# Optimization experiments

Hardware: AMD Instinct MI355X
Metric: run time of the kernel (lower is better)

The kernel has to match this reference:

```python
import jax, jax.numpy as jnp
import numpy as np

N_HEAD = 16

def _ln(x, g, b):
    m = jnp.mean(x, axis=-1, keepdims=True)
    v = jnp.var(x, axis=-1, keepdims=True)
    return (x - m) / jnp.sqrt(v + 1e-5) * g + b

def setup_inputs() -> dict:
    key = jax.random.key(0)
    B, T, D, L, V = 2, 1024, 1024, 4, 32000
    ks = jax.random.split(key, 8)
    s = 0.02
    return {
        'input_ids': jax.random.randint(ks[0], (B, T), 0, V),
        'wte': jax.random.normal(ks[1], (V, D), jnp.float32) * s,
        'wpe': jax.random.normal(ks[2], (T, D), jnp.float32) * s,
        'ln1_g': jnp.ones((L, D), jnp.float32), 'ln1_b': jnp.zeros((L, D), jnp.float32),
        'w_qkv': jax.random.normal(ks[3], (L, D, 3 * D), jnp.float32) * s,
        'b_qkv': jnp.zeros((L, 3 * D), jnp.float32),
        'w_proj': jax.random.normal(ks[4], (L, D, D), jnp.float32) * s,
        'b_proj': jnp.zeros((L, D), jnp.float32),
        'ln2_g': jnp.ones((L, D), jnp.float32), 'ln2_b': jnp.zeros((L, D), jnp.float32),
        'w_fc1': jax.random.normal(ks[5], (L, D, 4 * D), jnp.float32) * s,
        'b_fc1': jnp.zeros((L, 4 * D), jnp.float32),
        'w_fc2': jax.random.normal(ks[6], (L, 4 * D, D), jnp.float32) * s,
        'b_fc2': jnp.zeros((L, D), jnp.float32),
        'lnf_g': jnp.ones((D,), jnp.float32), 'lnf_b': jnp.zeros((D,), jnp.float32),
        'w_lm': jax.random.normal(ks[7], (D, V), jnp.float32) * s,
    }

def reference(input_ids, wte, wpe, ln1_g, ln1_b, w_qkv, b_qkv, w_proj, b_proj,
              ln2_g, ln2_b, w_fc1, b_fc1, w_fc2, b_fc2, lnf_g, lnf_b, w_lm):
    B, T = input_ids.shape
    D = wte.shape[1]
    H = N_HEAD
    hd = D // H
    mask = jnp.tril(jnp.ones((T, T), dtype=bool))  # causal
    x = wte[input_ids] + wpe[:T][None, :, :]  # token + position embeddings

    def layer(h, p):
        g1, bb1, Wq, bq, Wp, bp, g2, bb2, W1, b1, W2, b2 = p
        a = _ln(h, g1, bb1)
        qkv = a @ Wq + bq
        q, k, v = jnp.split(qkv, 3, axis=-1)
        q = q.reshape(B, T, H, hd)
        k = k.reshape(B, T, H, hd)
        v = v.reshape(B, T, H, hd)
        att = jnp.einsum('bqhd,bkhd->bhqk', q, k) / jnp.sqrt(jnp.float32(hd))
        att = jnp.where(mask[None, None], att, -jnp.inf)
        att = jax.nn.softmax(att, axis=-1)
        y = jnp.einsum('bhqk,bkhd->bqhd', att, v).reshape(B, T, D)
        h = h + y @ Wp + bp
        m = _ln(h, g2, bb2)
        # torch nn.GELU default is exact erf variant
        m = jax.nn.gelu(m @ W1 + b1, approximate=False) @ W2 + b2
        h = h + m
        return h, None

    params = (ln1_g, ln1_b, w_qkv, b_qkv, w_proj, b_proj,
              ln2_g, ln2_b, w_fc1, b_fc1, w_fc2, b_fc2)
    h, _ = jax.lax.scan(layer, x, params)
    h = _ln(h, lnf_g, lnf_b)
    logits = h @ w_lm  # [B, T, vocab]
    return logits
```

## Files before the change

### kernel.cpp

```cpp
#include <hip/hip_runtime.h>
#include <hip/hip_bf16.h>
#include <math.h>

typedef __attribute__((ext_vector_type(4))) float f32x4;
typedef __attribute__((ext_vector_type(8))) short short8;
typedef __attribute__((ext_vector_type(4))) unsigned short ushort4v;

__device__ __forceinline__ unsigned short f2bf(float f) {
    return __builtin_bit_cast(unsigned short, __float2bfloat16(f));
}

__device__ __forceinline__ void gload16(const void* g, void* l) {
    __builtin_amdgcn_global_load_lds(
        (const __attribute__((address_space(1))) unsigned int*)g,
        (__attribute__((address_space(3))) unsigned int*)l, 16, 0, 0);
}

__global__ __launch_bounds__(256)
void tc_kernel(const float* __restrict__ in, __hip_bfloat16* __restrict__ out,
               int N, int K)
{
    __shared__ float tile[64][65];
    const size_t loff = (size_t)blockIdx.z * K * N;
    const int k0 = blockIdx.x * 64, n0 = blockIdx.y * 64;
    const int t = threadIdx.x;
    {
        int kk = t >> 2, nb = (t & 3) * 16;
        const float* src = in + loff + (size_t)(k0 + kk) * N + n0 + nb;
        #pragma unroll
        for (int j = 0; j < 4; ++j) {
            float4 v = *(const float4*)(src + j * 4);
            tile[kk][nb + j*4 + 0] = v.x; tile[kk][nb + j*4 + 1] = v.y;
            tile[kk][nb + j*4 + 2] = v.z; tile[kk][nb + j*4 + 3] = v.w;
        }
    }
    __syncthreads();
    {
        int nn = t >> 2, kb = (t & 3) * 16;
        __hip_bfloat16* dst = out + loff + (size_t)(n0 + nn) * K + k0 + kb;
        short8 w0, w1;
        #pragma unroll
        for (int j = 0; j < 8; ++j) w0[j] = (short)f2bf(tile[kb + j][nn]);
        #pragma unroll
        for (int j = 0; j < 8; ++j) w1[j] = (short)f2bf(tile[kb + 8 + j][nn]);
        *(short8*)dst = w0;
        *(short8*)(dst + 8) = w1;
    }
}

__global__ __launch_bounds__(256)
void embed_kernel(const int* __restrict__ ids, const float* __restrict__ wte,
                  const float* __restrict__ wpe, float* __restrict__ h)
{
    int row  = blockIdx.x;
    int tpos = row & 1023;
    int id   = ids[row];
    float4 a = ((const float4*)(wte + (size_t)id * 1024))[threadIdx.x];
    float4 p = ((const float4*)(wpe + (size_t)tpos * 1024))[threadIdx.x];
    float4 o; o.x = a.x + p.x; o.y = a.y + p.y; o.z = a.z + p.z; o.w = a.w + p.w;
    ((float4*)(h + (size_t)row * 1024))[threadIdx.x] = o;
}

__global__ __launch_bounds__(256)
void ln_kernel(const float* __restrict__ x, const float* __restrict__ g,
               const float* __restrict__ b, __hip_bfloat16* __restrict__ out)
{
    size_t row = blockIdx.x;
    float4 v = ((const float4*)(x + row * 1024))[threadIdx.x];
    float s  = v.x + v.y + v.z + v.w;
    float s2 = v.x*v.x + v.y*v.y + v.z*v.z + v.w*v.w;
    #pragma unroll
    for (int off = 32; off; off >>= 1) {
        s  += __shfl_xor(s, off);
        s2 += __shfl_xor(s2, off);
    }
    __shared__ float rs[4], rs2[4];
    int wave = threadIdx.x >> 6;
    if ((threadIdx.x & 63) == 0) { rs[wave] = s; rs2[wave] = s2; }
    __syncthreads();
    s  = rs[0] + rs[1] + rs[2] + rs[3];
    s2 = rs2[0] + rs2[1] + rs2[2] + rs2[3];
    float mean = s * (1.f / 1024.f);
    float var  = s2 * (1.f / 1024.f) - mean * mean;
    float rstd = rsqrtf(var + 1e-5f);
    float4 gg = ((const float4*)g)[threadIdx.x];
    float4 bb = ((const float4*)b)[threadIdx.x];
    ushort4v ov;
    ov[0] = f2bf((v.x - mean) * rstd * gg.x + bb.x);
    ov[1] = f2bf((v.y - mean) * rstd * gg.y + bb.y);
    ov[2] = f2bf((v.z - mean) * rstd * gg.z + bb.z);
    ov[3] = f2bf((v.w - mean) * rstd * gg.w + bb.w);
    ((ushort4v*)(out + row * 1024))[threadIdx.x] = ov;
}

template<bool OUT_BF16, bool GELU_ACT, bool NT, int BN>
__global__ __launch_bounds__(256)
void gemm_bf16(const __hip_bfloat16* __restrict__ A,
               const __hip_bfloat16* __restrict__ Bt,
               const float* __restrict__ bias, const float* __restrict__ resid,
               void* __restrict__ Cout, int M, int N, int K, int GN)
{
    __shared__ unsigned char smem[32768 + 2 * BN * 128];
    int mblk, pnl;
    {
        int bid = blockIdx.x;
        int x = bid & 7, j = bid >> 3;
        int pw = GN >> 3;
        int whole = pw * 128;
        if (bid < whole) { pnl = x + 8 * (j >> 4); mblk = j & 15; }
        else { int r = bid - whole; pnl = (pw << 3) + (r >> 4); mblk = r & 15; }
    }
    const int m0 = mblk * 128;
    const int n0 = pnl * BN;
    const int t    = threadIdx.x;
    const int lane = t & 63;
    const int wave = t >> 6;
    constexpr int NF = (BN == 128) ? 4 : 2;
    const int wm = (BN == 128) ? (wave >> 1) * 64 : (wave & 1) * 64;
    const int wn = (BN == 128) ? (wave & 1) * 64 : (wave >> 1) * 32;

    f32x4 acc[4][NF];
    #pragma unroll
    for (int i = 0; i < 4; ++i)
        #pragma unroll
        for (int j = 0; j < NF; ++j) {
            acc[i][j][0] = 0.f; acc[i][j][1] = 0.f; acc[i][j][2] = 0.f; acc[i][j][3] = 0.f;
        }

    const int l8 = lane >> 3;
    const int lc = (lane & 7) ^ l8;
    constexpr int NB = NF;
    const __hip_bfloat16* agp[4];
    const __hip_bfloat16* bgp[NB];
    int aoff[4];
    int boff[NB];
    #pragma unroll
    for (int i = 0; i < 4; ++i) {
        int row = wave * 32 + i * 8 + l8;
        agp[i]  = A + (size_t)(m0 + row) * K + lc * 8;
        aoff[i] = (wave * 32 + i * 8) * 128;
    }
    #pragma unroll
    for (int i = 0; i < NB; ++i) {
        int row = wave * (BN / 4) + i * 8 + l8;
        bgp[i]  = Bt + (size_t)(n0 + row) * K + lc * 8;
        boff[i] = (wave * (BN / 4) + i * 8) * 128;
    }
    const int aBufOff[2] = { 0, 16384 };
    const int bBufOff[2] = { 32768, 32768 + BN * 128 };

    #pragma unroll
    for (int i = 0; i < 4; ++i)  gload16(agp[i], smem + aBufOff[0] + aoff[i]);
    #pragma unroll
    for (int i = 0; i < NB; ++i) gload16(bgp[i], smem + bBufOff[0] + boff[i]);
    __syncthreads();

    int cur = 0;
    for (int k0 = 0; k0 < K; k0 += 64) {
        if (k0 + 64 < K) {
            #pragma unroll
            for (int i = 0; i < 4; ++i)
                gload16(agp[i] + k0 + 64, smem + aBufOff[cur ^ 1] + aoff[i]);
            #pragma unroll
            for (int i = 0; i < NB; ++i)
                gload16(bgp[i] + k0 + 64, smem + bBufOff[cur ^ 1] + boff[i]);
        }
        const unsigned char* abuf = smem + aBufOff[cur];
        const unsigned char* bbuf = smem + bBufOff[cur];
        const int lr = lane & 15;
        const int lk = lane >> 4;
        #pragma unroll
        for (int ks = 0; ks < 2; ++ks) {
            int chunk = ks * 4 + lk;
            short8 af[4], bfr[NF];
            #pragma unroll
            for (int m = 0; m < 4; ++m) {
                int row = wm + m * 16 + lr;
                af[m] = *(const short8*)(abuf + row * 128 + ((chunk * 16) ^ ((row & 7) << 4)));
            }
            #pragma unroll
            for (int n = 0; n < NF; ++n) {
                int nn = wn + n * 16 + lr;
                bfr[n] = *(const short8*)(bbuf + nn * 128 + ((chunk * 16) ^ ((nn & 7) << 4)));
            }
            #pragma unroll
            for (int m = 0; m < 4; ++m)
                #pragma unroll
                for (int n = 0; n < NF; ++n)
                    acc[m][n] = __builtin_amdgcn_mfma_f32_16x16x32_bf16(af[m], bfr[n], acc[m][n], 0, 0, 0);
        }
        __syncthreads();
        cur ^= 1;
    }

    const int lr = lane & 15;
    const int lq = lane >> 4;
    float bv[NF];
    #pragma unroll
    for (int n = 0; n < NF; ++n)
        bv[n] = bias ? bias[n0 + wn + n * 16 + lr] : 0.f;
    #pragma unroll
    for (int m = 0; m < 4; ++m) {
        int rbase = m0 + wm + m * 16 + lq * 4;
        #pragma unroll
        for (int j = 0; j < 4; ++j) {
            int row = rbase + j;
            #pragma unroll
            for (int n = 0; n < NF; ++n) {
                int col = n0 + wn + n * 16 + lr;
                float v = acc[m][n][j] + bv[n];
                if (resid) v += resid[(size_t)row * N + col];
                if (GELU_ACT) v = 0.5f * v * (1.f + erff(v * 0.70710678118654752f));
                if (OUT_BF16) {
                    ((__hip_bfloat16*)Cout)[(size_t)row * N + col] = __float2bfloat16(v);
                } else if (NT) {
                    __builtin_nontemporal_store(v, (float*)Cout + (size_t)row * N + col);
                } else {
                    ((float*)Cout)[(size_t)row * N + col] = v;
                }
            }
        }
    }
}

__global__ __launch_bounds__(256)
void attn_mfma(const __hip_bfloat16* __restrict__ qkv,
               __hip_bfloat16* __restrict__ y)
{
    __shared__ short Qs[64][72];
    __shared__ short Ps[64][72];
    __shared__ unsigned char Kl[8192];
    __shared__ short Vt[64][72];

    const int bid = blockIdx.x;
    const int p   = bid >> 5;
    const int qt  = (p < 8) ? (15 - 2 * p) : (2 * (p - 8));
    const int bh  = bid & 31;
    const int b = bh >> 4, h = bh & 15;
    const int t = threadIdx.x, lane = t & 63, w = t >> 6;
    const int lr = lane & 15, lg = lane >> 4;
    const size_t base = (size_t)b * 1024 * 3072;
    const int qbase = qt * 64;

    {
        int row = t >> 2, c = t & 3;
        const short8* qsrc = (const short8*)(qkv + base + (size_t)(qbase + row) * 3072 + h * 64);
        *(short8*)&Qs[row][c * 8]      = qsrc[c];
        *(short8*)&Qs[row][c * 8 + 32] = qsrc[c + 4];
    }
    __syncthreads();

    short8 aq0 = *(const short8*)&Qs[w * 16 + lr][0 * 32 + lg * 8];
    short8 aq1 = *(const short8*)&Qs[w * 16 + lr][1 * 32 + lg * 8];

    f32x4 oacc[4];
    #pragma unroll
    for (int dt = 0; dt < 4; ++dt) { oacc[dt][0]=0.f; oacc[dt][1]=0.f; oacc[dt][2]=0.f; oacc[dt][3]=0.f; }
    float lsum[4] = {0.f, 0.f, 0.f, 0.f};

    const int ntiles = qt + 1;
    const int kkey = t >> 2, kc = t & 3;
    const int vkey = t & 63, vc = t >> 6;

    short8 rk0, rk1, rv0, rv1;
    {
        const short8* ksrc = (const short8*)(qkv + base + (size_t)kkey * 3072 + 1024 + h * 64);
        rk0 = ksrc[kc]; rk1 = ksrc[kc + 4];
        const short8* vsrc = (const short8*)(qkv + base + (size_t)vkey * 3072 + 2048 + h * 64);
        rv0 = vsrc[vc]; rv1 = vsrc[vc + 4];
    }
    {
        int rb = kkey * 128, sw = (kkey & 7) << 4;
        *(short8*)(Kl + rb + ((kc * 16) ^ sw)) = rk0;
        *(short8*)(Kl + rb + (((kc + 4) * 16) ^ sw)) = rk1;
        #pragma unroll
        for (int j = 0; j < 8; ++j) Vt[vc * 8 + j][vkey] = rv0[j];
        #pragma unroll
        for (int j = 0; j < 8; ++j) Vt[(vc + 4) * 8 + j][vkey] = rv1[j];
    }
    __syncthreads();

    for (int tile = 0; tile < ntiles; ++tile) {
        if (tile + 1 < ntiles) {
            const int kb2 = (tile + 1) * 64;
            const short8* ksrc = (const short8*)(qkv + base + (size_t)(kb2 + kkey) * 3072 + 1024 + h * 64);
            rk0 = ksrc[kc]; rk1 = ksrc[kc + 4];
            const short8* vsrc = (const short8*)(qkv + base + (size_t)(kb2 + vkey) * 3072 + 2048 + h * 64);
            rv0 = vsrc[vc]; rv1 = vsrc[vc + 4];
        }

        const int kb = tile * 64;
        f32x4 sacc[4];
        #pragma unroll
        for (int kt = 0; kt < 4; ++kt) { sacc[kt][0]=0.f; sacc[kt][1]=0.f; sacc[kt][2]=0.f; sacc[kt][3]=0.f; }
        #pragma unroll
        for (int ks = 0; ks < 2; ++ks) {
            short8 aq = ks ? aq1 : aq0;
            #pragma unroll
            for (int kt = 0; kt < 4; ++kt) {
                int krow = kt * 16 + lr;
                short8 bk = *(const short8*)(Kl + krow * 128 + (((ks * 4 + lg) * 16) ^ ((krow & 7) << 4)));
                sacc[kt] = __builtin_amdgcn_mfma_f32_16x16x32_bf16(aq, bk, sacc[kt], 0, 0, 0);
            }
        }

        #pragma unroll
        for (int kt = 0; kt < 4; ++kt) {
            int key = kb + kt * 16 + lr;
            #pragma unroll
            for (int j = 0; j < 4; ++j) {
                int q = qbase + w * 16 + lg * 4 + j;
                float pv = (key <= q) ? __expf(sacc[kt][j] * 0.125f) : 0.f;
                lsum[j] += pv;
                Ps[w * 16 + lg * 4 + j][kt * 16 + lr] = (short)f2bf(pv);
            }
        }

        #pragma unroll
        for (int ks = 0; ks < 2; ++ks) {
            short8 ap = *(const short8*)&Ps[w * 16 + lr][ks * 32 + lg * 8];
            #pragma unroll
            for (int dt = 0; dt < 4; ++dt) {
                short8 bv = *(const short8*)&Vt[dt * 16 + lr][ks * 32 + lg * 8];
                oacc[dt] = __builtin_amdgcn_mfma_f32_16x16x32_bf16(ap, bv, oacc[dt], 0, 0, 0);
            }
        }

        if (tile + 1 < ntiles) {
            __syncthreads();
            int rb = kkey * 128, sw = (kkey & 7) << 4;
            *(short8*)(Kl + rb + ((kc * 16) ^ sw)) = rk0;
            *(short8*)(Kl + rb + (((kc + 4) * 16) ^ sw)) = rk1;
            #pragma unroll
            for (int j = 0; j < 8; ++j) Vt[vc * 8 + j][vkey] = rv0[j];
            #pragma unroll
            for (int j = 0; j < 8; ++j) Vt[(vc + 4) * 8 + j][vkey] = rv1[j];
            __syncthreads();
        }
    }

    #pragma unroll
    for (int j = 0; j < 4; ++j) {
        float l = lsum[j];
        l += __shfl_xor(l, 1); l += __shfl_xor(l, 2);
        l += __shfl_xor(l, 4); l += __shfl_xor(l, 8);
        float inv = 1.f / l;
        int qrow = qbase + w * 16 + lg * 4 + j;
        __hip_bfloat16* dst = y + (size_t)(b * 1024 + qrow) * 1024 + h * 64;
        #pragma unroll
        for (int dt = 0; dt < 4; ++dt)
            dst[dt * 16 + lr] = __float2bfloat16(oacc[dt][j] * inv);
    }
}

extern "C" void kernel_launch(void* const* d_in, const int* in_sizes, int n_in,
                              void* d_out, int out_size, void* d_ws, size_t ws_size,
                              hipStream_t stream)
{
    (void)in_sizes; (void)n_in; (void)out_size; (void)ws_size;

    const int*   ids    = (const int*)d_in[0];
    const float* wte    = (const float*)d_in[1];
    const float* wpe    = (const float*)d_in[2];
    const float* ln1_g  = (const float*)d_in[3];
    const float* ln1_b  = (const float*)d_in[4];
    const float* w_qkv  = (const float*)d_in[5];
    const float* b_qkv  = (const float*)d_in[6];
    const float* w_proj = (const float*)d_in[7];
    const float* b_proj = (const float*)d_in[8];
    const float* ln2_g  = (const float*)d_in[9];
    const float* ln2_b  = (const float*)d_in[10];
    const float* w_fc1  = (const float*)d_in[11];
    const float* b_fc1  = (const float*)d_in[12];
    const float* w_fc2  = (const float*)d_in[13];
    const float* b_fc2  = (const float*)d_in[14];
    const float* lnf_g  = (const float*)d_in[15];
    const float* lnf_b  = (const float*)d_in[16];
    const float* w_lm   = (const float*)d_in[17];

    char* ws = (char*)d_ws;
    __hip_bfloat16* abuf_bf = (__hip_bfloat16*)ws;
    float*          hbuf    = (float*)(ws + (4u<<20));
    __hip_bfloat16* qkvb_bf = (__hip_bfloat16*)(ws + (12u<<20));
    __hip_bfloat16* ybuf_bf = (__hip_bfloat16*)(ws + (24u<<20));
    __hip_bfloat16* mbuf_bf = (__hip_bfloat16*)(ws + (28u<<20));
    __hip_bfloat16* wlm_bf  = (__hip_bfloat16*)(ws + (4u<<20));

    __hip_bfloat16* wq_bf = (__hip_bfloat16*)d_out;
    __hip_bfloat16* wp_bf = wq_bf + (size_t)4*1024*3072;
    __hip_bfloat16* w1_bf = wp_bf + (size_t)4*1024*1024;
    __hip_bfloat16* w2_bf = w1_bf + (size_t)4*1024*4096;

    float* out = (float*)d_out;

    tc_kernel<<<dim3(16, 48, 4), 256, 0, stream>>>(w_qkv,  wq_bf, 3072, 1024);
    tc_kernel<<<dim3(16, 16, 4), 256, 0, stream>>>(w_proj, wp_bf, 1024, 1024);
    tc_kernel<<<dim3(16, 64, 4), 256, 0, stream>>>(w_fc1,  w1_bf, 4096, 1024);
    tc_kernel<<<dim3(64, 16, 4), 256, 0, stream>>>(w_fc2,  w2_bf, 1024, 4096);

    embed_kernel<<<2048, 256, 0, stream>>>(ids, wte, wpe, hbuf);

    for (int l = 0; l < 4; ++l) {
        ln_kernel<<<2048, 256, 0, stream>>>(hbuf, ln1_g + l*1024, ln1_b + l*1024, abuf_bf);
        gemm_bf16<true,false,false,128><<<16*24, 256, 0, stream>>>(
            abuf_bf, wq_bf + (size_t)l*1024*3072, b_qkv + l*3072, nullptr, qkvb_bf, 2048, 3072, 1024, 24);
        attn_mfma<<<512, 256, 0, stream>>>(qkvb_bf, ybuf_bf);
        gemm_bf16<false,false,false,64><<<16*16, 256, 0, stream>>>(
            ybuf_bf, wp_bf + (size_t)l*1024*1024, b_proj + l*1024, hbuf, hbuf, 2048, 1024, 1024, 16);
        ln_kernel<<<2048, 256, 0, stream>>>(hbuf, ln2_g + l*1024, ln2_b + l*1024, abuf_bf);
        gemm_bf16<true,true,false,128><<<16*32, 256, 0, stream>>>(
            abuf_bf, w1_bf + (size_t)l*1024*4096, b_fc1 + l*4096, nullptr, mbuf_bf, 2048, 4096, 1024, 32);
        gemm_bf16<false,false,false,64><<<16*16, 256, 0, stream>>>(
            mbuf_bf, w2_bf + (size_t)l*4096*1024, b_fc2 + l*1024, hbuf, hbuf, 2048, 1024, 4096, 16);
    }

    ln_kernel<<<2048, 256, 0, stream>>>(hbuf, lnf_g, lnf_b, abuf_bf);
    tc_kernel<<<dim3(16, 500, 1), 256, 0, stream>>>(w_lm, wlm_bf, 32000, 1024);
    gemm_bf16<false,false,true,128><<<16*250, 256, 0, stream>>>(
        abuf_bf, wlm_bf, nullptr, nullptr, out, 2048, 32000, 1024, 250);
}
```

Measured before the change: 893.8 us.

## Triple-buffer GEMM LDS pipeline and use 128x64 tiles for all GEMMs

Switches the bf16 GEMM from double-buffered to triple-buffered LDS staging with two tiles in flight. Each iteration waits on vmcnt and issues one barrier instead of a full __syncthreads after compute. It also drops the BN=128 variant, so the QKV, FC1 and LM-head GEMMs now use 128x64 tiles with twice as many blocks. This should hide global-load latency better and raise block count, but LDS use grows to 72KB per block, which may lower occupancy. The narrower tiles also give less reuse of A per block.

```diff
diff --git a/kernel.cpp b/kernel.cpp
--- a/kernel.cpp
+++ b/kernel.cpp
@@ -15,6 +15,9 @@
         (const __attribute__((address_space(1))) unsigned int*)g,
         (__attribute__((address_space(3))) unsigned int*)l, 16, 0, 0);
 }
+
+#define WAITV6() asm volatile("s_waitcnt vmcnt(6)" ::: "memory")
+#define WAITV0() asm volatile("s_waitcnt vmcnt(0)" ::: "memory")
 
 __global__ __launch_bounds__(256)
 void tc_kernel(const float* __restrict__ in, __hip_bfloat16* __restrict__ out,
@@ -93,14 +96,14 @@
     ((ushort4v*)(out + row * 1024))[threadIdx.x] = ov;
 }
 
-template<bool OUT_BF16, bool GELU_ACT, bool NT, int BN>
+template<bool OUT_BF16, bool GELU_ACT, bool NT>
 __global__ __launch_bounds__(256)
 void gemm_bf16(const __hip_bfloat16* __restrict__ A,
                const __hip_bfloat16* __restrict__ Bt,
                const float* __restrict__ bias, const float* __restrict__ resid,
                void* __restrict__ Cout, int M, int N, int K, int GN)
 {
-    __shared__ unsigned char smem[32768 + 2 * BN * 128];
+    __shared__ unsigned char smem[73728];
     int mblk, pnl;
     {
         int bid = blockIdx.x;
@@ -111,29 +114,27 @@
         else { int r = bid - whole; pnl = (pw << 3) + (r >> 4); mblk = r & 15; }
     }
     const int m0 = mblk * 128;
-    const int n0 = pnl * BN;
+    const int n0 = pnl * 64;
     const int t    = threadIdx.x;
     const int lane = t & 63;
     const int wave = t >> 6;
-    constexpr int NF = (BN == 128) ? 4 : 2;
-    const int wm = (BN == 128) ? (wave >> 1) * 64 : (wave & 1) * 64;
-    const int wn = (BN == 128) ? (wave & 1) * 64 : (wave >> 1) * 32;
-
-    f32x4 acc[4][NF];
+    const int wm = (wave & 1) * 64;
+    const int wn = (wave >> 1) * 32;
+
+    f32x4 acc[4][2];
     #pragma unroll
     for (int i = 0; i < 4; ++i)
         #pragma unroll
-        for (int j = 0; j < NF; ++j) {
+        for (int j = 0; j < 2; ++j) {
             acc[i][j][0] = 0.f; acc[i][j][1] = 0.f; acc[i][j][2] = 0.f; acc[i][j][3] = 0.f;
         }
 
     const int l8 = lane >> 3;
     const int lc = (lane & 7) ^ l8;
-    constexpr int NB = NF;
     const __hip_bfloat16* agp[4];
-    const __hip_bfloat16* bgp[NB];
+    const __hip_bfloat16* bgp[2];
     int aoff[4];
-    int boff[NB];
+    int boff[2];
     #pragma unroll
     for (int i = 0; i < 4; ++i) {
         int row = wave * 32 + i * 8 + l8;
@@ -141,63 +142,68 @@
         aoff[i] = (wave * 32 + i * 8) * 128;
     }
     #pragma unroll
-    for (int i = 0; i < NB; ++i) {
-        int row = wave * (BN / 4) + i * 8 + l8;
+    for (int i = 0; i < 2; ++i) {
+        int row = wave * 16 + i * 8 + l8;
         bgp[i]  = Bt + (size_t)(n0 + row) * K + lc * 8;
-        boff[i] = (wave * (BN / 4) + i * 8) * 128;
-    }
-    const int aBufOff[2] = { 0, 16384 };
-    const int bBufOff[2] = { 32768, 32768 + BN * 128 };
-
-    #pragma unroll
-    for (int i = 0; i < 4; ++i)  gload16(agp[i], smem + aBufOff[0] + aoff[i]);
-    #pragma unroll
-    for (int i = 0; i < NB; ++i) gload16(bgp[i], smem + bBufOff[0] + boff[i]);
-    __syncthreads();
-
-    int cur = 0;
+        boff[i] = (wave * 16 + i * 8) * 128;
+    }
+
+    int a0 = 0,     a1 = 16384, a2 = 32768;
+    int b0 = 49152, b1 = 57344, b2 = 65536;
+
+    #pragma unroll
+    for (int i = 0; i < 4; ++i) gload16(agp[i], smem + a0 + aoff[i]);
+    #pragma unroll
+    for (int i = 0; i < 2; ++i) gload16(bgp[i], smem + b0 + boff[i]);
+    if (64 < K) {
+        #pragma unroll
+        for (int i = 0; i < 4; ++i) gload16(agp[i] + 64, smem + a1 + aoff[i]);
+        #pragma unroll
+        for (int i = 0; i < 2; ++i) gload16(bgp[i] + 64, smem + b1 + boff[i]);
+    }
+
     for (int k0 = 0; k0 < K; k0 += 64) {
-        if (k0 + 64 < K) {
-            #pragma unroll
-            for (int i = 0; i < 4; ++i)
-                gload16(agp[i] + k0 + 64, smem + aBufOff[cur ^ 1] + aoff[i]);
-            #pragma unroll
-            for (int i = 0; i < NB; ++i)
-                gload16(bgp[i] + k0 + 64, smem + bBufOff[cur ^ 1] + boff[i]);
-        }
-        const unsigned char* abuf = smem + aBufOff[cur];
-        const unsigned char* bbuf = smem + bBufOff[cur];
+        if (k0 + 64 < K) { WAITV6(); } else { WAITV0(); }
+        __builtin_amdgcn_s_barrier();
+        if (k0 + 128 < K) {
+            #pragma unroll
+            for (int i = 0; i < 4; ++i) gload16(agp[i] + k0 + 128, smem + a2 + aoff[i]);
+            #pragma unroll
+            for (int i = 0; i < 2; ++i) gload16(bgp[i] + k0 + 128, smem + b2 + boff[i]);
+        }
+        const unsigned char* abuf = smem + a0;
+        const unsigned char* bbuf = smem + b0;
         const int lr = lane & 15;
         const int lk = lane >> 4;
         #pragma unroll
         for (int ks = 0; ks < 2; ++ks) {
             int chunk = ks * 4 + lk;
-            short8 af[4], bfr[NF];
+            short8 af[4], bfr[2];
             #pragma unroll
             for (int m = 0; m < 4; ++m) {
                 int row = wm + m * 16 + lr;
                 af[m] = *(const short8*)(abuf + row * 128 + ((chunk * 16) ^ ((row & 7) << 4)));
             }
             #pragma unroll
-            for (int n = 0; n < NF; ++n) {
+            for (int n = 0; n < 2; ++n) {
                 int nn = wn + n * 16 + lr;
                 bfr[n] = *(const short8*)(bbuf + nn * 128 + ((chunk * 16) ^ ((nn & 7) << 4)));
             }
             #pragma unroll
             for (int m = 0; m < 4; ++m)
                 #pragma unroll
-                for (int n = 0; n < NF; ++n)
+                for (int n = 0; n < 2; ++n)
                     acc[m][n] = __builtin_amdgcn_mfma_f32_16x16x32_bf16(af[m], bfr[n], acc[m][n], 0, 0, 0);
         }
-        __syncthreads();
-        cur ^= 1;
+        int ta = a0; a0 = a1; a1 = a2; a2 = ta;
+        int tb = b0; b0 = b1; b1 = b2; b2 = tb;
     }
 
     const int lr = lane & 15;
     const int lq = lane >> 4;
-    float bv[NF];
-    #pragma unroll
-    for (int n = 0; n < NF; ++n)
+    float bv[2];
+    #pragma unroll
+    for (int n = 0; n < 2; ++n)
         bv[n] = bias ? bias[n0 + wn + n * 16 + lr] : 0.f;
     #pragma unroll
     for (int m = 0; m < 4; ++m) {
@@ -206,7 +212,7 @@
         for (int j = 0; j < 4; ++j) {
             int row = rbase + j;
             #pragma unroll
-            for (int n = 0; n < NF; ++n) {
+            for (int n = 0; n < 2; ++n) {
                 int col = n0 + wn + n * 16 + lr;
                 float v = acc[m][n][j] + bv[n];
                 if (resid) v += resid[(size_t)row * N + col];
@@ -402,20 +408,20 @@
 
     for (int l = 0; l < 4; ++l) {
         ln_kernel<<<2048, 256, 0, stream>>>(hbuf, ln1_g + l*1024, ln1_b + l*1024, abuf_bf);
-        gemm_bf16<true,false,false,128><<<16*24, 256, 0, stream>>>(
-            abuf_bf, wq_bf + (size_t)l*1024*3072, b_qkv + l*3072, nullptr, qkvb_bf, 2048, 3072, 1024, 24);
+        gemm_bf16<true,false,false><<<16*48, 256, 0, stream>>>(
+            abuf_bf, wq_bf + (size_t)l*1024*3072, b_qkv + l*3072, nullptr, qkvb_bf, 2048, 3072, 1024, 48);
         attn_mfma<<<512, 256, 0, stream>>>(qkvb_bf, ybuf_bf);
-        gemm_bf16<false,false,false,64><<<16*16, 256, 0, stream>>>(
+        gemm_bf16<false,false,false><<<16*16, 256, 0, stream>>>(
             ybuf_bf, wp_bf + (size_t)l*1024*1024, b_proj + l*1024, hbuf, hbuf, 2048, 1024, 1024, 16);
         ln_kernel<<<2048, 256, 0, stream>>>(hbuf, ln2_g + l*1024, ln2_b + l*1024, abuf_bf);
-        gemm_bf16<true,true,false,128><<<16*32, 256, 0, stream>>>(
-            abuf_bf, w1_bf + (size_t)l*1024*4096, b_fc1 + l*4096, nullptr, mbuf_bf, 2048, 4096, 1024, 32);
-        gemm_bf16<false,false,false,64><<<16*16, 256, 0, stream>>>(
+        gemm_bf16<true,true,false><<<16*64, 256, 0, stream>>>(
+            abuf_bf, w1_bf + (size_t)l*1024*4096, b_fc1 + l*4096, nullptr, mbuf_bf, 2048, 4096, 1024, 64);
+        gemm_bf16<false,false,false><<<16*16, 256, 0, stream>>>(
             mbuf_bf, w2_bf + (size_t)l*4096*1024, b_fc2 + l*1024, hbuf, hbuf, 2048, 1024, 4096, 16);
     }
 
     ln_kernel<<<2048, 256, 0, stream>>>(hbuf, lnf_g, lnf_b, abuf_bf);
     tc_kernel<<<dim3(16, 500, 1), 256, 0, stream>>>(w_lm, wlm_bf, 32000, 1024);
-    gemm_bf16<false,false,true,128><<<16*250, 256, 0, stream>>>(
-        abuf_bf, wlm_bf, nullptr, nullptr, out, 2048, 32000, 1024, 250);
-}
+    gemm_bf16<false,false,true><<<16*500, 256, 0, stream>>>(
+        abuf_bf, wlm_bf, nullptr, nullptr, out, 2048, 32000, 1024, 500);
+}
```

Result: faster. 850.3 us (-4.9%).
